# Optimization experiments

Hardware: AMD Instinct MI355X
Metric: run time of the kernel (lower is better)

## Reference

```python
import jax, jax.numpy as jnp
import numpy as np

DIM = 1024
NUM_HEADS = 16
HEAD_DIM = DIM // NUM_HEADS
SCALE = HEAD_DIM ** (-0.5)


def setup_inputs() -> dict:
    key = jax.random.key(0)
    ks = jax.random.split(key, 5)
    B, L, D = 2, 2048, DIM
    x = jax.random.normal(ks[0], (B, L, D), dtype=jnp.float32)
    # torch nn.Linear init scale ~ U(-1/sqrt(fan_in), 1/sqrt(fan_in)); use small normals
    s = 1.0 / np.sqrt(D)
    qkv_w = jax.random.uniform(ks[1], (3 * D, D), minval=-s, maxval=s, dtype=jnp.float32)
    qkv_b = jax.random.uniform(ks[2], (3 * D,), minval=-s, maxval=s, dtype=jnp.float32)
    proj_w = jax.random.uniform(ks[3], (D, D), minval=-s, maxval=s, dtype=jnp.float32)
    proj_b = jax.random.uniform(ks[4], (D,), minval=-s, maxval=s, dtype=jnp.float32)
    return {"x": x, "qkv_w": qkv_w, "qkv_b": qkv_b, "proj_w": proj_w, "proj_b": proj_b}


def reference(x, qkv_w, qkv_b, proj_w, proj_b):
    B, L, D = x.shape
    H, Hd = NUM_HEADS, HEAD_DIM
    # QKV projection: [B,L,3D] -> [3,B,H,L,Hd]
    qkv = x @ qkv_w.T + qkv_b
    qkv = qkv.reshape(B, L, 3, H, Hd).transpose(2, 0, 3, 1, 4)
    q, k, v = qkv[0], qkv[1], qkv[2]
    scores = jnp.einsum('bhqd,bhkd->bhqk', q, k) * SCALE  # [B,H,L,L]
    attn = jax.nn.softmax(scores, axis=-1)
    out = jnp.einsum('bhqk,bhkd->bhqd', attn, v)  # [B,H,L,Hd]
    out = out.transpose(0, 2, 1, 3).reshape(B, L, D)
    out = out @ proj_w.T + proj_b
    return out
```

## Files before the change

kernel.cpp:

```cpp
#include <hip/hip_runtime.h>
#include <hip/hip_bf16.h>
#include <cstdint>
#include <cstddef>

#define D_MODEL 1024
#define NHEADS 16
#define HD 64
#define NB 2
#define SL 2048
#define SEQ (NB*SL)
#define NQKV (3*D_MODEL)

typedef __attribute__((ext_vector_type(8))) short short8;
typedef __attribute__((ext_vector_type(4))) float floatx4;
typedef unsigned short u16;

__device__ __forceinline__ u16 f2bf(float f) {
    union { float f; uint32_t u; } v; v.f = f;
    return (u16)((v.u + 0x7fffu + ((v.u >> 16) & 1u)) >> 16);
}

__global__ __launch_bounds__(256) void cvt_kernel(const float* __restrict__ in,
                                                  u16* __restrict__ out, int n4) {
    int i = blockIdx.x * 256 + threadIdx.x;
    if (i >= n4) return;
    float4 f = ((const float4*)in)[i];
    ushort4 o;
    o.x = f2bf(f.x); o.y = f2bf(f.y); o.z = f2bf(f.z); o.w = f2bf(f.w);
    ((ushort4*)out)[i] = o;
}

__device__ __forceinline__ void gemm128_staged(const u16* __restrict__ A,
                                               const u16* __restrict__ B,
                                               int mbase, int nbase, int K,
                                               u16* Alds, u16* Blds,
                                               floatx4 acc[4][4]) {
    const int tid = threadIdx.x;
    const int lane = tid & 63;
    const int l15 = lane & 15, quad = lane >> 4;
    const int wave = tid >> 6;
    const int wr = wave >> 1, wc = wave & 1;
    #pragma unroll
    for (int i = 0; i < 4; i++)
        #pragma unroll
        for (int j = 0; j < 4; j++)
            acc[i][j] = (floatx4){0.f, 0.f, 0.f, 0.f};

    const int r0 = tid >> 2, kg0 = (tid & 3) * 8;
    const int r1 = (256 + tid) >> 2, kg1 = kg0;
    const u16* Arow0 = A + (size_t)(mbase + r0) * K + kg0;
    const u16* Arow1 = A + (size_t)(mbase + r1) * K + kg1;
    const u16* Brow0 = B + (size_t)(nbase + r0) * K + kg0;
    const u16* Brow1 = B + (size_t)(nbase + r1) * K + kg1;

    for (int k0 = 0; k0 < K; k0 += 32) {
        __syncthreads();
        __builtin_amdgcn_global_load_lds(
            (const __attribute__((address_space(1))) void*)(Arow0 + k0),
            (__attribute__((address_space(3))) void*)(Alds + tid * 8), 16, 0, 0);
        __builtin_amdgcn_global_load_lds(
            (const __attribute__((address_space(1))) void*)(Arow1 + k0),
            (__attribute__((address_space(3))) void*)(Alds + (256 + tid) * 8), 16, 0, 0);
        __builtin_amdgcn_global_load_lds(
            (const __attribute__((address_space(1))) void*)(Brow0 + k0),
            (__attribute__((address_space(3))) void*)(Blds + tid * 8), 16, 0, 0);
        __builtin_amdgcn_global_load_lds(
            (const __attribute__((address_space(1))) void*)(Brow1 + k0),
            (__attribute__((address_space(3))) void*)(Blds + (256 + tid) * 8), 16, 0, 0);
        __syncthreads();

        short8 af[4], bf[4];
        #pragma unroll
        for (int i = 0; i < 4; i++)
            af[i] = *(const short8*)(Alds + (wr * 64 + i * 16 + l15) * 32 + quad * 8);
        #pragma unroll
        for (int j = 0; j < 4; j++)
            bf[j] = *(const short8*)(Blds + (wc * 64 + j * 16 + l15) * 32 + quad * 8);
        #pragma unroll
        for (int i = 0; i < 4; i++)
            #pragma unroll
            for (int j = 0; j < 4; j++)
                acc[i][j] = __builtin_amdgcn_mfma_f32_16x16x32_bf16(af[i], bf[j], acc[i][j], 0, 0, 0);
    }
}

__global__ __launch_bounds__(256) void qkv_gemm(const u16* __restrict__ xb,
                                                const u16* __restrict__ wb,
                                                const float* __restrict__ bias,
                                                u16* __restrict__ Qo, u16* __restrict__ Ko,
                                                u16* __restrict__ Vt) {
    __shared__ __align__(16) u16 Alds[128 * 32];
    __shared__ __align__(16) u16 Blds[128 * 32];
    const int mbase = blockIdx.y * 128;
    const int nbase = blockIdx.x * 128;
    floatx4 acc[4][4];
    gemm128_staged(xb, wb, mbase, nbase, 1024, Alds, Blds, acc);
    const int lane = threadIdx.x & 63;
    const int wave = threadIdx.x >> 6;
    const int wr = wave >> 1, wc = wave & 1;
    const int l15 = lane & 15, quad = lane >> 4;
    #pragma unroll
    for (int j = 0; j < 4; j++) {
        int n = nbase + wc * 64 + j * 16 + l15;
        float bv = bias[n];
        int which = n >> 10;
        int within = n & 1023;
        int h = within >> 6, d = within & 63;
        #pragma unroll
        for (int i = 0; i < 4; i++) {
            #pragma unroll
            for (int r = 0; r < 4; r++) {
                int m = mbase + wr * 64 + i * 16 + quad * 4 + r;
                int b = m >> 11, l = m & 2047;
                int bh = b * NHEADS + h;
                float v = acc[i][j][r] + bv;
                if (which == 0)      Qo[((size_t)bh * SL + l) * HD + d] = f2bf(v * 0.125f);
                else if (which == 1) Ko[((size_t)bh * SL + l) * HD + d] = f2bf(v);
                else                 Vt[((size_t)bh * HD + d) * SL + l] = f2bf(v);
            }
        }
    }
}

#define KSTR 72
#define VSTR 136
#define PSTRIDE 136
__global__ __launch_bounds__(256) void flash_kernel(const u16* __restrict__ Q,
                                                    const u16* __restrict__ K,
                                                    const u16* __restrict__ V,
                                                    u16* __restrict__ AO) {
    __shared__ __align__(16) u16 Klds[128 * KSTR];
    __shared__ __align__(16) u16 Vlds[64 * VSTR];
    __shared__ __align__(16) u16 pbuf[4][16][PSTRIDE];
    const int tid = threadIdx.x;
    const int wave = tid >> 6;
    const int lane = tid & 63;
    const int l15 = lane & 15, quad = lane >> 4;
    const int bh = blockIdx.y;
    const int b = bh >> 4, h = bh & 15;
    const int qbase = blockIdx.x * 64 + wave * 16;
    const u16* Qp = Q + (size_t)bh * SL * HD;
    const u16* Kp = K + (size_t)bh * SL * HD;
    const u16* Vp = V + (size_t)bh * HD * SL;

    short8 qf0 = *(const short8*)(Qp + (size_t)(qbase + l15) * HD + quad * 8);
    short8 qf1 = *(const short8*)(Qp + (size_t)(qbase + l15) * HD + 32 + quad * 8);

    floatx4 accO[4];
    #pragma unroll
    for (int d = 0; d < 4; d++) accO[d] = (floatx4){0.f, 0.f, 0.f, 0.f};
    float m_i = -__builtin_inff();
    float l_i = 0.f;

    for (int kt = 0; kt < SL; kt += 128) {
        short8 kreg[4], vreg[4];
        #pragma unroll
        for (int it = 0; it < 4; it++) {
            int c = it * 256 + tid;
            kreg[it] = *(const short8*)(Kp + (size_t)(kt + (c >> 3)) * HD + (c & 7) * 8);
        }
        #pragma unroll
        for (int it = 0; it < 4; it++) {
            int c = it * 256 + tid;
            vreg[it] = *(const short8*)(Vp + (size_t)(c >> 4) * SL + kt + (c & 15) * 8);
        }
        __syncthreads();
        #pragma unroll
        for (int it = 0; it < 4; it++) {
            int c = it * 256 + tid;
            *(short8*)(&Klds[(c >> 3) * KSTR + (c & 7) * 8]) = kreg[it];
        }
        #pragma unroll
        for (int it = 0; it < 4; it++) {
            int c = it * 256 + tid;
            *(short8*)(&Vlds[(c >> 4) * VSTR + (c & 15) * 8]) = vreg[it];
        }
        __syncthreads();

        floatx4 s[8];
        #pragma unroll
        for (int j = 0; j < 8; j++) {
            const u16* kr = &Klds[(j * 16 + l15) * KSTR + quad * 8];
            short8 ka = *(const short8*)(kr);
            short8 kb = *(const short8*)(kr + 32);
            floatx4 z = (floatx4){0.f, 0.f, 0.f, 0.f};
            z = __builtin_amdgcn_mfma_f32_16x16x32_bf16(ka, qf0, z, 0, 0, 0);
            s[j] = __builtin_amdgcn_mfma_f32_16x16x32_bf16(kb, qf1, z, 0, 0, 0);
        }
        float mx = s[0][0];
        #pragma unroll
        for (int j = 0; j < 8; j++)
            #pragma unroll
            for (int r = 0; r < 4; r++) mx = fmaxf(mx, s[j][r]);
        mx = fmaxf(mx, __shfl_xor(mx, 16, 64));
        mx = fmaxf(mx, __shfl_xor(mx, 32, 64));
        float mnew = fmaxf(m_i, mx);
        float alpha = __expf(m_i - mnew);
        m_i = mnew;
        float rs = 0.f;
        #pragma unroll
        for (int j = 0; j < 8; j++) {
            float p0 = __expf(s[j][0] - mnew);
            float p1 = __expf(s[j][1] - mnew);
            float p2 = __expf(s[j][2] - mnew);
            float p3 = __expf(s[j][3] - mnew);
            rs += (p0 + p1) + (p2 + p3);
            ushort4 pk;
            pk.x = f2bf(p0); pk.y = f2bf(p1); pk.z = f2bf(p2); pk.w = f2bf(p3);
            *(ushort4*)(&pbuf[wave][l15][j * 16 + quad * 4]) = pk;
        }
        rs += __shfl_xor(rs, 16, 64);
        rs += __shfl_xor(rs, 32, 64);
        l_i = l_i * alpha + rs;
        #pragma unroll
        for (int r = 0; r < 4; r++) {
            float a_r = __shfl(alpha, quad * 4 + r, 16);
            #pragma unroll
            for (int d = 0; d < 4; d++) accO[d][r] *= a_r;
        }
        #pragma unroll
        for (int ks = 0; ks < 4; ks++) {
            short8 pf = *(const short8*)(&pbuf[wave][l15][ks * 32 + quad * 8]);
            #pragma unroll
            for (int d = 0; d < 4; d++) {
                short8 vf = *(const short8*)(&Vlds[(d * 16 + l15) * VSTR + ks * 32 + quad * 8]);
                accO[d] = __builtin_amdgcn_mfma_f32_16x16x32_bf16(pf, vf, accO[d], 0, 0, 0);
            }
        }
    }
    float invl = 1.f / l_i;
    #pragma unroll
    for (int r = 0; r < 4; r++) {
        float inv_r = __shfl(invl, quad * 4 + r, 16);
        int row = b * SL + qbase + quad * 4 + r;
        #pragma unroll
        for (int d = 0; d < 4; d++) {
            int col = h * HD + d * 16 + l15;
            AO[(size_t)row * D_MODEL + col] = f2bf(accO[d][r] * inv_r);
        }
    }
}

__global__ __launch_bounds__(256) void proj_gemm(const u16* __restrict__ ab,
                                                 const u16* __restrict__ wb,
                                                 const float* __restrict__ bias,
                                                 float* __restrict__ out) {
    __shared__ __align__(16) u16 Alds[128 * 32];
    __shared__ __align__(16) u16 Blds[128 * 32];
    const int mbase = blockIdx.y * 128;
    const int nbase = blockIdx.x * 128;
    floatx4 acc[4][4];
    gemm128_staged(ab, wb, mbase, nbase, 1024, Alds, Blds, acc);
    const int lane = threadIdx.x & 63;
    const int wave = threadIdx.x >> 6;
    const int wr = wave >> 1, wc = wave & 1;
    const int l15 = lane & 15, quad = lane >> 4;
    #pragma unroll
    for (int j = 0; j < 4; j++) {
        int n = nbase + wc * 64 + j * 16 + l15;
        float bv = bias[n];
        #pragma unroll
        for (int i = 0; i < 4; i++) {
            #pragma unroll
            for (int r = 0; r < 4; r++) {
                int m = mbase + wr * 64 + i * 16 + quad * 4 + r;
                out[(size_t)m * D_MODEL + n] = acc[i][j][r] + bv;
            }
        }
    }
}

extern "C" void kernel_launch(void* const* d_in, const int* in_sizes, int n_in,
                              void* d_out, int out_size, void* d_ws, size_t ws_size,
                              hipStream_t stream) {
    const float* x      = (const float*)d_in[0];
    const float* qkv_w  = (const float*)d_in[1];
    const float* qkv_b  = (const float*)d_in[2];
    const float* proj_w = (const float*)d_in[3];
    const float* proj_b = (const float*)d_in[4];
    float* out = (float*)d_out;
    char* ws = (char*)d_ws;

    u16* xb    = (u16*)(ws);
    u16* wqkv  = (u16*)(ws + 8388608);
    u16* wproj = (u16*)(ws + 14680064);
    u16* Qb    = (u16*)(ws + 16777216);
    u16* Kb    = (u16*)(ws + 25165824);
    u16* Vt    = (u16*)(ws + 33554432);
    u16* AO    = (u16*)(ws + 41943040);

    cvt_kernel<<<4096, 256, 0, stream>>>(x, xb, 4194304 / 4);
    cvt_kernel<<<3072, 256, 0, stream>>>(qkv_w, wqkv, 3145728 / 4);
    cvt_kernel<<<1024, 256, 0, stream>>>(proj_w, wproj, 1048576 / 4);
    qkv_gemm<<<dim3(NQKV / 128, SEQ / 128), 256, 0, stream>>>(xb, wqkv, qkv_b, Qb, Kb, Vt);
    flash_kernel<<<dim3(SL / 64, NB * NHEADS), 256, 0, stream>>>(Qb, Kb, Vt, AO);
    proj_gemm<<<dim3(D_MODEL / 128, SEQ / 128), 256, 0, stream>>>(AO, wproj, proj_b, out);
}
```

Before: 232.2 us.

## Rewrite flash attention with 32x32 MFMA, pre-tiled K/V layout and double-buffered LDS

```diff
diff --git a/kernel.cpp b/kernel.cpp
--- a/kernel.cpp
+++ b/kernel.cpp
@@ -13,12 +13,34 @@
 
 typedef __attribute__((ext_vector_type(8))) short short8;
 typedef __attribute__((ext_vector_type(4))) float floatx4;
+typedef __attribute__((ext_vector_type(16))) float f32x16;
 typedef unsigned short u16;
 
 __device__ __forceinline__ u16 f2bf(float f) {
     union { float f; uint32_t u; } v; v.f = f;
     return (u16)((v.u + 0x7fffu + ((v.u >> 16) & 1u)) >> 16);
 }
+
+__device__ __forceinline__ uint32_t cvt_pk_bf16(float lo, float hi) {
+    uint32_t r;
+    asm("v_cvt_pk_bf16_f32 %0, %1, %2" : "=v"(r) : "v"(lo), "v"(hi));
+    return r;
+}
+
+__device__ __forceinline__ void pl32swap(uint32_t &a, uint32_t &b) {
+    asm("v_permlane32_swap_b32 %0, %1" : "+v"(a), "+v"(b));
+}
+
+__device__ __forceinline__ f32x16 zero16() {
+    f32x16 z;
+    #pragma unroll
+    for (int i = 0; i < 16; i++) z[i] = 0.f;
+    return z;
+}
+
+#define GLDS(gsrc, ldst) __builtin_amdgcn_global_load_lds( \
+    (const __attribute__((address_space(1))) void*)(gsrc), \
+    (__attribute__((address_space(3))) void*)(ldst), 16, 0, 0)
 
 __global__ __launch_bounds__(256) void cvt_kernel(const float* __restrict__ in,
                                                   u16* __restrict__ out, int n4) {
@@ -55,18 +77,10 @@
 
     for (int k0 = 0; k0 < K; k0 += 32) {
         __syncthreads();
-        __builtin_amdgcn_global_load_lds(
-            (const __attribute__((address_space(1))) void*)(Arow0 + k0),
-            (__attribute__((address_space(3))) void*)(Alds + tid * 8), 16, 0, 0);
-        __builtin_amdgcn_global_load_lds(
-            (const __attribute__((address_space(1))) void*)(Arow1 + k0),
-            (__attribute__((address_space(3))) void*)(Alds + (256 + tid) * 8), 16, 0, 0);
-        __builtin_amdgcn_global_load_lds(
-            (const __attribute__((address_space(1))) void*)(Brow0 + k0),
-            (__attribute__((address_space(3))) void*)(Blds + tid * 8), 16, 0, 0);
-        __builtin_amdgcn_global_load_lds(
-            (const __attribute__((address_space(1))) void*)(Brow1 + k0),
-            (__attribute__((address_space(3))) void*)(Blds + (256 + tid) * 8), 16, 0, 0);
+        GLDS(Arow0 + k0, Alds + tid * 8);
+        GLDS(Arow1 + k0, Alds + (256 + tid) * 8);
+        GLDS(Brow0 + k0, Blds + tid * 8);
+        GLDS(Brow1 + k0, Blds + (256 + tid) * 8);
         __syncthreads();
 
         short8 af[4], bf[4];
@@ -114,130 +128,138 @@
                 int b = m >> 11, l = m & 2047;
                 int bh = b * NHEADS + h;
                 float v = acc[i][j][r] + bv;
-                if (which == 0)      Qo[((size_t)bh * SL + l) * HD + d] = f2bf(v * 0.125f);
-                else if (which == 1) Ko[((size_t)bh * SL + l) * HD + d] = f2bf(v);
-                else                 Vt[((size_t)bh * HD + d) * SL + l] = f2bf(v);
+                if (which == 0) {
+                    Qo[((size_t)bh * SL + l) * HD + d] = f2bf(v * 0.125f);
+                } else if (which == 1) {
+                    int slot = ((l >> 5) & 1) * 256 + (d >> 4) * 64 + ((d >> 3) & 1) * 32 + (l & 31);
+                    Ko[(size_t)bh * (SL * HD) + (size_t)(l >> 6) * 4096 + slot * 8 + (d & 7)] = f2bf(v);
+                } else {
+                    int slot = ((l >> 5) & 1) * 256 + ((l >> 4) & 1) * 128 + (d >> 5) * 64 + ((l >> 3) & 1) * 32 + (d & 31);
+                    Vt[(size_t)bh * (SL * HD) + (size_t)(l >> 6) * 4096 + slot * 8 + (l & 7)] = f2bf(v);
+                }
             }
         }
     }
 }
 
-#define KSTR 72
-#define VSTR 136
-#define PSTRIDE 136
-__global__ __launch_bounds__(256) void flash_kernel(const u16* __restrict__ Q,
-                                                    const u16* __restrict__ K,
-                                                    const u16* __restrict__ V,
-                                                    u16* __restrict__ AO) {
-    __shared__ __align__(16) u16 Klds[128 * KSTR];
-    __shared__ __align__(16) u16 Vlds[64 * VSTR];
-    __shared__ __align__(16) u16 pbuf[4][16][PSTRIDE];
+__global__ __launch_bounds__(256, 2) void flash_kernel(const u16* __restrict__ Q,
+                                                       const u16* __restrict__ K,
+                                                       const u16* __restrict__ V,
+                                                       u16* __restrict__ AO) {
+    __shared__ __align__(16) u16 Klds[2 * 4096];
+    __shared__ __align__(16) u16 Vlds[2 * 4096];
     const int tid = threadIdx.x;
+    const int lane = tid & 63;
     const int wave = tid >> 6;
-    const int lane = tid & 63;
-    const int l15 = lane & 15, quad = lane >> 4;
-    const int bh = blockIdx.y;
+    const int hi = lane >> 5;
+    const int l31 = lane & 31;
+    const int lane8 = lane * 8;
+
+    const int bid = (int)blockIdx.x;
+    const int swz = (bid & 7) * 64 + (bid >> 3);
+    const int bh = swz >> 4;
+    const int qb = swz & 15;
     const int b = bh >> 4, h = bh & 15;
-    const int qbase = blockIdx.x * 64 + wave * 16;
+    const int qbase = qb * 128 + wave * 32;
+
     const u16* Qp = Q + (size_t)bh * SL * HD;
-    const u16* Kp = K + (size_t)bh * SL * HD;
-    const u16* Vp = V + (size_t)bh * HD * SL;
-
-    short8 qf0 = *(const short8*)(Qp + (size_t)(qbase + l15) * HD + quad * 8);
-    short8 qf1 = *(const short8*)(Qp + (size_t)(qbase + l15) * HD + 32 + quad * 8);
-
-    floatx4 accO[4];
-    #pragma unroll
-    for (int d = 0; d < 4; d++) accO[d] = (floatx4){0.f, 0.f, 0.f, 0.f};
+    const u16* Kg = K + (size_t)bh * (SL * HD);
+    const u16* Vg = V + (size_t)bh * (SL * HD);
+
+    short8 qf[4];
+    #pragma unroll
+    for (int c = 0; c < 4; c++)
+        qf[c] = *(const short8*)(Qp + (size_t)(qbase + l31) * HD + c * 16 + hi * 8);
+
+    f32x16 accO0 = zero16(), accO1 = zero16();
     float m_i = -__builtin_inff();
     float l_i = 0.f;
 
-    for (int kt = 0; kt < SL; kt += 128) {
-        short8 kreg[4], vreg[4];
-        #pragma unroll
-        for (int it = 0; it < 4; it++) {
-            int c = it * 256 + tid;
-            kreg[it] = *(const short8*)(Kp + (size_t)(kt + (c >> 3)) * HD + (c & 7) * 8);
-        }
-        #pragma unroll
-        for (int it = 0; it < 4; it++) {
-            int c = it * 256 + tid;
-            vreg[it] = *(const short8*)(Vp + (size_t)(c >> 4) * SL + kt + (c & 15) * 8);
-        }
-        __syncthreads();
-        #pragma unroll
-        for (int it = 0; it < 4; it++) {
-            int c = it * 256 + tid;
-            *(short8*)(&Klds[(c >> 3) * KSTR + (c & 7) * 8]) = kreg[it];
-        }
-        #pragma unroll
-        for (int it = 0; it < 4; it++) {
-            int c = it * 256 + tid;
-            *(short8*)(&Vlds[(c >> 4) * VSTR + (c & 15) * 8]) = vreg[it];
-        }
-        __syncthreads();
-
-        floatx4 s[8];
-        #pragma unroll
-        for (int j = 0; j < 8; j++) {
-            const u16* kr = &Klds[(j * 16 + l15) * KSTR + quad * 8];
-            short8 ka = *(const short8*)(kr);
-            short8 kb = *(const short8*)(kr + 32);
-            floatx4 z = (floatx4){0.f, 0.f, 0.f, 0.f};
-            z = __builtin_amdgcn_mfma_f32_16x16x32_bf16(ka, qf0, z, 0, 0, 0);
-            s[j] = __builtin_amdgcn_mfma_f32_16x16x32_bf16(kb, qf1, z, 0, 0, 0);
-        }
-        float mx = s[0][0];
-        #pragma unroll
-        for (int j = 0; j < 8; j++)
-            #pragma unroll
-            for (int r = 0; r < 4; r++) mx = fmaxf(mx, s[j][r]);
-        mx = fmaxf(mx, __shfl_xor(mx, 16, 64));
+    GLDS(Kg + tid * 8,         Klds + tid * 8);
+    GLDS(Kg + (256 + tid) * 8, Klds + (256 + tid) * 8);
+    GLDS(Vg + tid * 8,         Vlds + tid * 8);
+    GLDS(Vg + (256 + tid) * 8, Vlds + (256 + tid) * 8);
+    __syncthreads();
+
+    union PW { uint32_t w[4]; short8 s8; };
+
+    for (int t = 0; t < SL / 64; t++) {
+        const int cur = t & 1;
+        if (t + 1 < SL / 64) {
+            const u16* ks = Kg + (size_t)(t + 1) * 4096;
+            const u16* vs = Vg + (size_t)(t + 1) * 4096;
+            u16* kd = Klds + (cur ^ 1) * 4096;
+            u16* vd = Vlds + (cur ^ 1) * 4096;
+            GLDS(ks + tid * 8,         kd + tid * 8);
+            GLDS(ks + (256 + tid) * 8, kd + (256 + tid) * 8);
+            GLDS(vs + tid * 8,         vd + tid * 8);
+            GLDS(vs + (256 + tid) * 8, vd + (256 + tid) * 8);
+        }
+        const u16* Kt  = Klds + cur * 4096;
+        const u16* Vt_ = Vlds + cur * 4096;
+
+        f32x16 sA = zero16(), sB = zero16();
+        #pragma unroll
+        for (int c = 0; c < 4; c++) {
+            short8 kf = *(const short8*)(Kt + c * 512 + lane8);
+            sA = __builtin_amdgcn_mfma_f32_32x32x16_bf16(kf, qf[c], sA, 0, 0, 0);
+        }
+        #pragma unroll
+        for (int c = 0; c < 4; c++) {
+            short8 kf = *(const short8*)(Kt + 2048 + c * 512 + lane8);
+            sB = __builtin_amdgcn_mfma_f32_32x32x16_bf16(kf, qf[c], sB, 0, 0, 0);
+        }
+
+        float mx = fmaxf(sA[0], sA[1]);
+        #pragma unroll
+        for (int e = 2; e < 16; e++) mx = fmaxf(mx, sA[e]);
+        #pragma unroll
+        for (int e = 0; e < 16; e++) mx = fmaxf(mx, sB[e]);
         mx = fmaxf(mx, __shfl_xor(mx, 32, 64));
-        float mnew = fmaxf(m_i, mx);
-        float alpha = __expf(m_i - mnew);
+        const float mnew = fmaxf(m_i, mx);
+        const float alpha = __expf(m_i - mnew);
         m_i = mnew;
         float rs = 0.f;
         #pragma unroll
-        for (int j = 0; j < 8; j++) {
-            float p0 = __expf(s[j][0] - mnew);
-            float p1 = __expf(s[j][1] - mnew);
-            float p2 = __expf(s[j][2] - mnew);
-            float p3 = __expf(s[j][3] - mnew);
-            rs += (p0 + p1) + (p2 + p3);
-            ushort4 pk;
-            pk.x = f2bf(p0); pk.y = f2bf(p1); pk.z = f2bf(p2); pk.w = f2bf(p3);
-            *(ushort4*)(&pbuf[wave][l15][j * 16 + quad * 4]) = pk;
-        }
-        rs += __shfl_xor(rs, 16, 64);
+        for (int e = 0; e < 16; e++) { float p = __expf(sA[e] - mnew); sA[e] = p; rs += p; }
+        #pragma unroll
+        for (int e = 0; e < 16; e++) { float p = __expf(sB[e] - mnew); sB[e] = p; rs += p; }
         rs += __shfl_xor(rs, 32, 64);
         l_i = l_i * alpha + rs;
         #pragma unroll
-        for (int r = 0; r < 4; r++) {
-            float a_r = __shfl(alpha, quad * 4 + r, 16);
-            #pragma unroll
-            for (int d = 0; d < 4; d++) accO[d][r] *= a_r;
-        }
-        #pragma unroll
-        for (int ks = 0; ks < 4; ks++) {
-            short8 pf = *(const short8*)(&pbuf[wave][l15][ks * 32 + quad * 8]);
-            #pragma unroll
-            for (int d = 0; d < 4; d++) {
-                short8 vf = *(const short8*)(&Vlds[(d * 16 + l15) * VSTR + ks * 32 + quad * 8]);
-                accO[d] = __builtin_amdgcn_mfma_f32_16x16x32_bf16(pf, vf, accO[d], 0, 0, 0);
-            }
-        }
-    }
-    float invl = 1.f / l_i;
-    #pragma unroll
-    for (int r = 0; r < 4; r++) {
-        float inv_r = __shfl(invl, quad * 4 + r, 16);
-        int row = b * SL + qbase + quad * 4 + r;
-        #pragma unroll
-        for (int d = 0; d < 4; d++) {
-            int col = h * HD + d * 16 + l15;
-            AO[(size_t)row * D_MODEL + col] = f2bf(accO[d][r] * inv_r);
-        }
+        for (int e = 0; e < 16; e++) { accO0[e] *= alpha; accO1[e] *= alpha; }
+
+#define PV_SUB(SV, OFF) { \
+        uint32_t a0 = cvt_pk_bf16(SV[0], SV[1]);  uint32_t b0 = cvt_pk_bf16(SV[4], SV[5]);  pl32swap(a0, b0); \
+        uint32_t a1 = cvt_pk_bf16(SV[2], SV[3]);  uint32_t b1 = cvt_pk_bf16(SV[6], SV[7]);  pl32swap(a1, b1); \
+        PW f0; f0.w[0] = a0; f0.w[1] = a1; f0.w[2] = b0; f0.w[3] = b1; \
+        accO0 = __builtin_amdgcn_mfma_f32_32x32x16_bf16(*(const short8*)(Vt_ + (OFF) + lane8),        f0.s8, accO0, 0, 0, 0); \
+        accO1 = __builtin_amdgcn_mfma_f32_32x32x16_bf16(*(const short8*)(Vt_ + (OFF) + 512 + lane8),  f0.s8, accO1, 0, 0, 0); \
+        uint32_t c0 = cvt_pk_bf16(SV[8], SV[9]);  uint32_t d0 = cvt_pk_bf16(SV[12], SV[13]); pl32swap(c0, d0); \
+        uint32_t c1 = cvt_pk_bf16(SV[10], SV[11]); uint32_t d1 = cvt_pk_bf16(SV[14], SV[15]); pl32swap(c1, d1); \
+        PW f1; f1.w[0] = c0; f1.w[1] = c1; f1.w[2] = d0; f1.w[3] = d1; \
+        accO0 = __builtin_amdgcn_mfma_f32_32x32x16_bf16(*(const short8*)(Vt_ + (OFF) + 1024 + lane8),       f1.s8, accO0, 0, 0, 0); \
+        accO1 = __builtin_amdgcn_mfma_f32_32x32x16_bf16(*(const short8*)(Vt_ + (OFF) + 1024 + 512 + lane8), f1.s8, accO1, 0, 0, 0); }
+
+        PV_SUB(sA, 0);
+        PV_SUB(sB, 2048);
+#undef PV_SUB
+
+        __syncthreads();
+    }
+
+    const float invl = 1.f / l_i;
+    const int qrow = qbase + l31;
+    const size_t rowbase = ((size_t)(b * SL + qrow)) * D_MODEL + h * HD;
+    #pragma unroll
+    for (int rg = 0; rg < 4; rg++) {
+        ushort4 o0, o1;
+        o0.x = f2bf(accO0[rg * 4 + 0] * invl); o0.y = f2bf(accO0[rg * 4 + 1] * invl);
+        o0.z = f2bf(accO0[rg * 4 + 2] * invl); o0.w = f2bf(accO0[rg * 4 + 3] * invl);
+        *(ushort4*)(AO + rowbase + rg * 8 + 4 * hi) = o0;
+        o1.x = f2bf(accO1[rg * 4 + 0] * invl); o1.y = f2bf(accO1[rg * 4 + 1] * invl);
+        o1.z = f2bf(accO1[rg * 4 + 2] * invl); o1.w = f2bf(accO1[rg * 4 + 3] * invl);
+        *(ushort4*)(AO + rowbase + 32 + rg * 8 + 4 * hi) = o1;
     }
 }
 
@@ -293,6 +315,6 @@
     cvt_kernel<<<3072, 256, 0, stream>>>(qkv_w, wqkv, 3145728 / 4);
     cvt_kernel<<<1024, 256, 0, stream>>>(proj_w, wproj, 1048576 / 4);
     qkv_gemm<<<dim3(NQKV / 128, SEQ / 128), 256, 0, stream>>>(xb, wqkv, qkv_b, Qb, Kb, Vt);
-    flash_kernel<<<dim3(SL / 64, NB * NHEADS), 256, 0, stream>>>(Qb, Kb, Vt, AO);
+    flash_kernel<<<dim3(512), 256, 0, stream>>>(Qb, Kb, Vt, AO);
     proj_gemm<<<dim3(D_MODEL / 128, SEQ / 128), 256, 0, stream>>>(AO, wproj, proj_b, out);
 }
```

After: 219.7 us. -5.4%, faster.
